# Optimization experiments

Hardware: AMD Instinct MI355X
Metric: run time of the kernel (lower is better)

## Reference

```python
import jax, jax.numpy as jnp
import numpy as np

# Dims (match init_kwargs / input_specs)
B, S, HID = 1, 2048, 2048
NH, NKV, HD = 16, 4, 128          # head_dim = HID // NH
REP = NH // NKV                    # num_key_value_groups
BLOCK_SIZE, LOCAL_BLOCKS, SINK_NUM = 8, 4, 4
SCALING = HD ** -0.5


def rotate_half(x):
    x1, x2 = jnp.split(x, 2, axis=-1)
    return jnp.concatenate([-x2, x1], axis=-1)


def setup_inputs() -> dict:
    key = jax.random.key(0)
    ks = jax.random.split(key, 7)
    return {
        "hidden_states": jax.random.normal(ks[0], (B, S, HID), jnp.float32),
        "cos": jax.random.uniform(ks[1], (B, S, HD), jnp.float32, minval=-1.0, maxval=1.0),
        "sin": jax.random.uniform(ks[2], (B, S, HD), jnp.float32, minval=-1.0, maxval=1.0),
        # Projection weights stored as [in, out] so x @ W matches nn.Linear (bias=False).
        "Wq": 0.02 * jax.random.normal(ks[3], (HID, NH * HD), jnp.float32),
        "Wk": 0.02 * jax.random.normal(ks[4], (HID, NKV * HD), jnp.float32),
        "Wv": 0.02 * jax.random.normal(ks[5], (HID, NKV * HD), jnp.float32),
        "Wo": 0.02 * jax.random.normal(ks[6], (NH * HD, HID), jnp.float32),
    }


def sink_local_mask(seq_len):
    # query i attends to: sink tokens j < min(SINK_NUM, i), and local window
    # max(0, i - LOCAL_BLOCKS*BLOCK_SIZE) <= j <= i (diagonal included so every
    # row has at least one valid key; see notes).
    i = jnp.arange(seq_len)[:, None]
    j = jnp.arange(seq_len)[None, :]
    sink = j < jnp.minimum(SINK_NUM, i)
    local = (j >= i - LOCAL_BLOCKS * BLOCK_SIZE) & (j <= i)
    return sink | local  # [S, S] bool, broadcast over (B, H)


def reference(hidden_states, cos, sin, Wq, Wk, Wv, Wo):
    # projections -> [B, H, S, D]
    q = (hidden_states @ Wq).reshape(B, S, NH, HD).transpose(0, 2, 1, 3)
    k = (hidden_states @ Wk).reshape(B, S, NKV, HD).transpose(0, 2, 1, 3)
    v = (hidden_states @ Wv).reshape(B, S, NKV, HD).transpose(0, 2, 1, 3)
    # rotary embedding, cos/sin broadcast over head dim (unsqueeze_dim=1)
    c = cos[:, None, :, :]
    s = sin[:, None, :, :]
    q = q * c + rotate_half(q) * s
    k = k * c + rotate_half(k) * s
    # repeat_kv (GQA) -> [B, NH, S, D]
    k = jnp.repeat(k, REP, axis=1)
    v = jnp.repeat(v, REP, axis=1)
    # sink + local sparse attention (dense compute + mask, as in source)
    scores = jnp.einsum('bhqd,bhkd->bhqk', q, k) * SCALING
    mask = sink_local_mask(S)
    scores = jnp.where(mask, scores, -jnp.inf)
    attn_weights = jax.nn.softmax(scores, axis=-1)
    attn_output = jnp.einsum('bhqk,bhkd->bhqd', attn_weights, v)
    # Faithful to source: view(B, S, -1) on the [B, H, S, D] layout WITHOUT a
    # transpose(1,2) first (the original code omits it).
    attn_output = attn_output.reshape(B, S, NH * HD)
    attn_output = attn_output @ Wo
    return attn_output, attn_weights
```

## Files before the change

kernel.cpp:

```cpp
#include <hip/hip_runtime.h>

typedef unsigned short ushort_t;
typedef __attribute__((ext_vector_type(8))) short short8;
typedef __attribute__((ext_vector_type(4))) float f32x4;
typedef __attribute__((ext_vector_type(8))) unsigned short us8;
typedef __attribute__((ext_vector_type(4))) unsigned short us4;

#define SEQ 2048
#define HIDD 2048
#define XLD 3072
#define SCALING 0.08838834764831843f

__device__ __forceinline__ float bf2f(ushort_t u) {
    unsigned int x = ((unsigned int)u) << 16;
    return __builtin_bit_cast(float, x);
}
__device__ __forceinline__ ushort_t f2bf(float f) {
    unsigned int u = __builtin_bit_cast(unsigned int, f);
    u += 0x7fffu + ((u >> 16) & 1u);
    return (ushort_t)(u >> 16);
}

__device__ __forceinline__ void transpose_tile(
    const float* __restrict__ W, ushort_t* __restrict__ Wt,
    int N, int n0, int k0, int dstRow0) {
    __shared__ ushort_t t[64 * 80];
    const int tid = threadIdx.x;
    {
        const int kl = tid >> 4;
        const int nc = (tid & 15) * 4;
        #pragma unroll
        for (int p = 0; p < 4; ++p) {
            int k = kl + p * 16;
            float4 v = *(const float4*)(W + (size_t)(k0 + k) * N + n0 + nc);
            t[(nc + 0) * 80 + k] = f2bf(v.x);
            t[(nc + 1) * 80 + k] = f2bf(v.y);
            t[(nc + 2) * 80 + k] = f2bf(v.z);
            t[(nc + 3) * 80 + k] = f2bf(v.w);
        }
    }
    __syncthreads();
    {
        const int nl = tid >> 3;
        const int kc = (tid & 7) * 8;
        #pragma unroll
        for (int p = 0; p < 2; ++p) {
            int n = nl + p * 32;
            *(us8*)(Wt + (size_t)(dstRow0 + n) * HIDD + k0 + kc) =
                *(const us8*)&t[n * 80 + kc];
        }
    }
}

__global__ __launch_bounds__(256) void transpose_all(
    const float* __restrict__ Wq, const float* __restrict__ Wk,
    const float* __restrict__ Wv, const float* __restrict__ Wo,
    const float* __restrict__ hid,
    ushort_t* __restrict__ Wqkvt, ushort_t* __restrict__ Wot,
    ushort_t* __restrict__ Hb) {
    int bx = blockIdx.x, k0 = blockIdx.y * 64;
    if (bx < 32)       transpose_tile(Wq, Wqkvt, 2048, bx * 64,        k0, bx * 64);
    else if (bx < 40)  transpose_tile(Wk, Wqkvt, 512,  (bx - 32) * 64, k0, 2048 + (bx - 32) * 64);
    else if (bx < 48)  transpose_tile(Wv, Wqkvt, 512,  (bx - 40) * 64, k0, 2560 + (bx - 40) * 64);
    else if (bx < 80)  transpose_tile(Wo, Wot,   2048, (bx - 48) * 64, k0, (bx - 48) * 64);
    else {
        int chunk = (bx - 80) * 32 + blockIdx.y;
        size_t base = (size_t)chunk * 4096 + threadIdx.x * 16;
        #pragma unroll
        for (int p = 0; p < 4; ++p) {
            float4 v = *(const float4*)(hid + base + p * 4);
            us4 o;
            o[0] = f2bf(v.x); o[1] = f2bf(v.y); o[2] = f2bf(v.z); o[3] = f2bf(v.w);
            *(us4*)(Hb + base + p * 4) = o;
        }
    }
}

__global__ __launch_bounds__(256) void gemm_splitk(
    const ushort_t* __restrict__ A, int lda,
    const ushort_t* __restrict__ Bt, int ldb,
    ushort_t* __restrict__ P, int ldc,
    const int4 kexts) {
    __shared__ ushort_t lA[2 * 128 * 32];
    __shared__ ushort_t lB[2 * 128 * 32];
    const int tid = threadIdx.x;
    const int wave = tid >> 6, lane = tid & 63;
    const int wm = wave >> 1, wn = wave & 1;
    const int quad = lane >> 4, l16 = lane & 15;
    const int m0 = blockIdx.y * 128, n0 = blockIdx.x * 128;
    const int z = blockIdx.z;

    const int ke[4] = {kexts.x, kexts.y, kexts.z, kexts.w};
    int koff = 0;
    for (int zz = 0; zz < 4; ++zz) if (zz < z) koff += ke[zz];
    const int kext = ke[z];

    A  += (size_t)koff;
    Bt += (size_t)koff;
    P  += (size_t)z * ((size_t)gridDim.y * 128) * ldc;

    const int srow = lane >> 2;
    const int scol = 8 * ((lane & 3) ^ (srow & 3));

    f32x4 acc[4][4] = {};

    const ushort_t* Ab = A  + (size_t)(m0 + wave * 16 + srow) * lda + scol;
    const ushort_t* Bb = Bt + (size_t)(n0 + wave * 16 + srow) * ldb + scol;
    ushort_t* lAw = lA + (wave * 16) * 32;
    ushort_t* lBw = lB + (wave * 16) * 32;

    const int rsw = (quad ^ (l16 & 3)) * 8;

    for (int kk = 0; kk < kext; kk += 64) {
        __syncthreads();
        #pragma unroll
        for (int kh = 0; kh < 2; ++kh) {
            #pragma unroll
            for (int c = 0; c < 2; ++c) {
                __builtin_amdgcn_global_load_lds(
                    (const __attribute__((address_space(1))) unsigned int*)(const void*)
                        (Ab + (size_t)(c * 64) * lda + kk + kh * 32),
                    (__attribute__((address_space(3))) unsigned int*)(void*)
                        (lAw + kh * 128 * 32 + c * 64 * 32), 16, 0, 0);
                __builtin_amdgcn_global_load_lds(
                    (const __attribute__((address_space(1))) unsigned int*)(const void*)
                        (Bb + (size_t)(c * 64) * ldb + kk + kh * 32),
                    (__attribute__((address_space(3))) unsigned int*)(void*)
                        (lBw + kh * 128 * 32 + c * 64 * 32), 16, 0, 0);
            }
        }
        __syncthreads();
        #pragma unroll
        for (int kh = 0; kh < 2; ++kh) {
            short8 af[4], bfr[4];
            #pragma unroll
            for (int mt = 0; mt < 4; ++mt)
                af[mt] = *(const short8*)&lA[kh * 128 * 32 + (wm * 64 + mt * 16 + l16) * 32 + rsw];
            #pragma unroll
            for (int nt = 0; nt < 4; ++nt)
                bfr[nt] = *(const short8*)&lB[kh * 128 * 32 + (wn * 64 + nt * 16 + l16) * 32 + rsw];
            #pragma unroll
            for (int mt = 0; mt < 4; ++mt) {
                #pragma unroll
                for (int nt = 0; nt < 4; ++nt)
                    acc[mt][nt] = __builtin_amdgcn_mfma_f32_16x16x32_bf16(
                        af[mt], bfr[nt], acc[mt][nt], 0, 0, 0);
            }
        }
    }

    #pragma unroll
    for (int mt = 0; mt < 4; ++mt) {
        #pragma unroll
        for (int nt = 0; nt < 4; ++nt) {
            int gm = m0 + wm * 64 + mt * 16 + quad * 4;
            int gn = n0 + wn * 64 + nt * 16 + l16;
            #pragma unroll
            for (int r = 0; r < 4; ++r)
                P[(size_t)(gm + r) * ldc + gn] = f2bf(acc[mt][nt][r]);
        }
    }
}

#define RWAVES (SEQ * 10)
#define VWAVES (SEQ * 2)
__global__ __launch_bounds__(256) void reduce_x(
    const ushort_t* __restrict__ P, ushort_t* __restrict__ X,
    const float* __restrict__ cosp, const float* __restrict__ sinp) {
    const size_t ZS = (size_t)SEQ * XLD;
    int wid = blockIdx.x * 4 + (threadIdx.x >> 6);
    int lane = threadIdx.x & 63;
    if (wid < RWAVES) {
        int s = wid / 10, seg = wid % 10;
        int c0 = seg * 256 + lane * 4;
        size_t base = (size_t)s * XLD + c0;
        us4 a = *(const us4*)(P + base);
        us4 b = *(const us4*)(P + ZS + base);
        float x[4];
        #pragma unroll
        for (int t = 0; t < 4; ++t) x[t] = bf2f(a[t]) + bf2f(b[t]);
        float p[4];
        #pragma unroll
        for (int t = 0; t < 4; ++t) p[t] = __shfl_xor(x[t], 16, 64);
        int d = (lane * 4) & 127;
        float4 cv = *(const float4*)(cosp + (size_t)s * 128 + d);
        float4 sv = *(const float4*)(sinp + (size_t)s * 128 + d);
        float sgn = (lane & 16) ? 1.f : -1.f;
        us4 o;
        o[0] = f2bf(x[0] * cv.x + sgn * p[0] * sv.x);
        o[1] = f2bf(x[1] * cv.y + sgn * p[1] * sv.y);
        o[2] = f2bf(x[2] * cv.z + sgn * p[2] * sv.z);
        o[3] = f2bf(x[3] * cv.w + sgn * p[3] * sv.w);
        *(us4*)(X + base) = o;
    } else {
        int w2 = wid - RWAVES;
        int s = w2 >> 1;
        int c0 = 2560 + (w2 & 1) * 256 + lane * 4;
        size_t base = (size_t)s * XLD + c0;
        us4 a = *(const us4*)(P + base);
        us4 b = *(const us4*)(P + ZS + base);
        us4 o;
        #pragma unroll
        for (int t = 0; t < 4; ++t) o[t] = f2bf(bf2f(a[t]) + bf2f(b[t]));
        *(us4*)(X + base) = o;
    }
}

__global__ __launch_bounds__(256) void reduce_out3(
    const ushort_t* __restrict__ P, float* __restrict__ out) {
    const size_t ZS = (size_t)SEQ * HIDD;
    size_t idx = ((size_t)blockIdx.x * 256 + threadIdx.x) * 4;
    us4 a = *(const us4*)(P + idx);
    us4 b = *(const us4*)(P + ZS + idx);
    us4 c = *(const us4*)(P + 2 * ZS + idx);
    float4 o;
    o.x = bf2f(a[0]) + bf2f(b[0]) + bf2f(c[0]);
    o.y = bf2f(a[1]) + bf2f(b[1]) + bf2f(c[1]);
    o.z = bf2f(a[2]) + bf2f(b[2]) + bf2f(c[2]);
    o.w = bf2f(a[3]) + bf2f(b[3]) + bf2f(c[3]);
    *(float4*)(out + idx) = o;
}

__device__ __forceinline__ float qk_round(
    const ushort_t* __restrict__ Kbase, const float* qf,
    int jg, int dg, int lo, int nsink, int r) {
    int jj = r * 16 + jg;
    int j = (jj < nsink) ? jj : (lo + jj - nsink);
    if (j > SEQ - 1) j = SEQ - 1;
    const uint4* kp = (const uint4*)(Kbase + (size_t)j * XLD + dg * 32);
    float p = 0.f;
    #pragma unroll
    for (int pq = 0; pq < 4; ++pq) {
        uint4 v = kp[pq];
        unsigned int uu[4] = {v.x, v.y, v.z, v.w};
        #pragma unroll
        for (int t = 0; t < 4; ++t) {
            p += qf[pq * 8 + t * 2]     * bf2f((ushort_t)(uu[t] & 0xffffu));
            p += qf[pq * 8 + t * 2 + 1] * bf2f((ushort_t)(uu[t] >> 16));
        }
    }
    p += __shfl_xor(p, 1, 64);
    p += __shfl_xor(p, 2, 64);
    return p * SCALING;
}

__global__ __launch_bounds__(256) void attn_kernel(
    const ushort_t* __restrict__ X, float* __restrict__ Wts,
    ushort_t* __restrict__ Aout) {
    int g = blockIdx.x * 4 + (threadIdx.x >> 6);
    int lane = threadIdx.x & 63;
    int i = g & (SEQ - 1);
    int h = g >> 11;

    const int dg = lane & 3;
    const int jg = lane >> 2;

    const ushort_t* Q = X + (size_t)i * XLD + h * 128;
    float qf[32];
    {
        const uint4* qp = (const uint4*)(Q + dg * 32);
        #pragma unroll
        for (int p = 0; p < 4; ++p) {
            uint4 v = qp[p];
            unsigned int uu[4] = {v.x, v.y, v.z, v.w};
            #pragma unroll
            for (int t = 0; t < 4; ++t) {
                qf[p * 8 + t * 2]     = bf2f((ushort_t)(uu[t] & 0xffffu));
                qf[p * 8 + t * 2 + 1] = bf2f((ushort_t)(uu[t] >> 16));
            }
        }
    }

    int lo = i - 32; if (lo < 0) lo = 0;
    int nsink = lo < 4 ? lo : 4;
    int NJ = nsink + (i - lo + 1);

    const ushort_t* Kbase = X + 2048 + (h >> 2) * 128;
    const ushort_t* Vbase = X + 2560 + (h >> 2) * 128;

    float s0 = qk_round(Kbase, qf, jg, dg, lo, nsink, 0);
    float s1 = qk_round(Kbase, qf, jg, dg, lo, nsink, 1);
    float s2 = qk_round(Kbase, qf, jg, dg, lo, nsink, 2);

    int src = (lane & 15) * 4;
    float m0 = __shfl(s0, src, 64);
    float m1 = __shfl(s1, src, 64);
    float m2 = __shfl(s2, src, 64);
    float mysc = (lane < 16) ? m0 : ((lane < 32) ? m1 : m2);
    if (lane >= NJ) mysc = -1e30f;

    float m = mysc;
    #pragma unroll
    for (int off = 32; off > 0; off >>= 1) m = fmaxf(m, __shfl_xor(m, off, 64));

    float e = (lane < NJ) ? expf(mysc - m) : 0.f;
    float l = e;
    #pragma unroll
    for (int off = 32; off > 0; off >>= 1) l += __shfl_xor(l, off, 64);
    float w = e / l;

    float* row = Wts + ((size_t)h * SEQ + i) * SEQ;
    #pragma unroll
    for (int s = 0; s < 8; ++s) {
        float4 o;
        #pragma unroll
        for (int t = 0; t < 4; ++t) {
            int c = s * 256 + lane * 4 + t;
            bool in = (c < nsink) || (c >= lo && c <= i);
            int jjc = in ? ((c < nsink) ? c : (nsink + c - lo)) : 0;
            float wv = __shfl(w, jjc, 64);
            o[t] = in ? wv : 0.f;
        }
        *(float4*)(row + s * 256 + lane * 4) = o;
    }

    float o0 = 0.f, o1 = 0.f;
    for (int jj = 0; jj < NJ; ++jj) {
        int j = (jj < nsink) ? jj : (lo + jj - nsink);
        float pb = __shfl(w, jj, 64);
        unsigned int vv = *(const unsigned int*)(Vbase + (size_t)j * XLD + 2 * lane);
        o0 += pb * bf2f((ushort_t)(vv & 0xffff));
        o1 += pb * bf2f((ushort_t)(vv >> 16));
    }
    int r = h * 128 + (i >> 4);
    int c = (i & 15) * 128 + 2 * lane;
    ushort_t* Ar = Aout + (size_t)r * HIDD + c;
    Ar[0] = f2bf(o0);
    Ar[1] = f2bf(o1);
}

extern "C" void kernel_launch(void* const* d_in, const int* in_sizes, int n_in,
                              void* d_out, int out_size, void* d_ws, size_t ws_size,
                              hipStream_t stream) {
    if (n_in < 7) return;
    const float* hid  = (const float*)d_in[0];
    const float* cosp = (const float*)d_in[1];
    const float* sinp = (const float*)d_in[2];
    const float* Wq   = (const float*)d_in[3];
    const float* Wk   = (const float*)d_in[4];
    const float* Wv   = (const float*)d_in[5];
    const float* Wo   = (const float*)d_in[6];

    float* out = (float*)d_out;
    float* wts = out + (size_t)SEQ * HIDD;

    ushort_t* Hb    = (ushort_t*)d_ws;
    ushort_t* Wqkvt = Hb    + (size_t)2048 * 2048;
    ushort_t* Wot   = Wqkvt + (size_t)3072 * 2048;
    ushort_t* X     = Wot   + (size_t)2048 * 2048;
    ushort_t* Am    = X     + (size_t)SEQ * XLD;
    ushort_t* Pqkv  = Am    + (size_t)SEQ * HIDD;
    ushort_t* Pout  = Pqkv  + 2 * (size_t)SEQ * XLD;
    size_t need = ((char*)(Pout + 3 * (size_t)SEQ * HIDD)) - (char*)d_ws;
    if (ws_size < need) return;

    dim3 blk(256);
    transpose_all<<<dim3(112, 32), blk, 0, stream>>>(
        Wq, Wk, Wv, Wo, hid, Wqkvt, Wot, Hb);

    gemm_splitk<<<dim3(24, 16, 2), blk, 0, stream>>>(
        Hb, HIDD, Wqkvt, 2048, Pqkv, XLD, make_int4(1024, 1024, 0, 0));
    reduce_x<<<(RWAVES + VWAVES) / 4, blk, 0, stream>>>(
        Pqkv, X, cosp, sinp);

    attn_kernel<<<(SEQ * 16) / 4, blk, 0, stream>>>(X, wts, Am);

    gemm_splitk<<<dim3(16, 16, 3), blk, 0, stream>>>(
        Am, HIDD, Wot, 2048, Pout, HIDD, make_int4(704, 704, 640, 0));
    reduce_out3<<<(SEQ * HIDD) / (256 * 4), blk, 0, stream>>>(Pout, out);
}
```

Baseline: 492.3 us.

## Stage shared K/V window in LDS for blocks of 16 queries

```diff
diff --git a/kernel.cpp b/kernel.cpp
--- a/kernel.cpp
+++ b/kernel.cpp
@@ -221,23 +221,25 @@
     *(float4*)(out + idx) = o;
 }
 
-__device__ __forceinline__ float qk_round(
-    const ushort_t* __restrict__ Kbase, const float* qf,
-    int jg, int dg, int lo, int nsink, int r) {
+#define SMLD 136
+__device__ __forceinline__ float qk_round_lds(
+    const ushort_t* __restrict__ sm, const float* qf,
+    int jg, int dg, int lo, int nsink, int w0, int r) {
     int jj = r * 16 + jg;
-    int j = (jj < nsink) ? jj : (lo + jj - nsink);
-    if (j > SEQ - 1) j = SEQ - 1;
-    const uint4* kp = (const uint4*)(Kbase + (size_t)j * XLD + dg * 32);
+    int row;
+    if (jj < nsink) row = 48 + jj;
+    else {
+        int widx = lo + jj - nsink - w0;
+        if (widx > 47) widx = 47;
+        row = widx;
+    }
+    const ushort_t* kp = sm + row * SMLD + dg * 32;
     float p = 0.f;
     #pragma unroll
     for (int pq = 0; pq < 4; ++pq) {
-        uint4 v = kp[pq];
-        unsigned int uu[4] = {v.x, v.y, v.z, v.w};
-        #pragma unroll
-        for (int t = 0; t < 4; ++t) {
-            p += qf[pq * 8 + t * 2]     * bf2f((ushort_t)(uu[t] & 0xffffu));
-            p += qf[pq * 8 + t * 2 + 1] * bf2f((ushort_t)(uu[t] >> 16));
-        }
+        us8 v = *(const us8*)(kp + pq * 8);
+        #pragma unroll
+        for (int t = 0; t < 8; ++t) p += qf[pq * 8 + t] * bf2f(v[t]);
     }
     p += __shfl_xor(p, 1, 64);
     p += __shfl_xor(p, 2, 64);
@@ -247,86 +249,106 @@
 __global__ __launch_bounds__(256) void attn_kernel(
     const ushort_t* __restrict__ X, float* __restrict__ Wts,
     ushort_t* __restrict__ Aout) {
-    int g = blockIdx.x * 4 + (threadIdx.x >> 6);
-    int lane = threadIdx.x & 63;
-    int i = g & (SEQ - 1);
-    int h = g >> 11;
+    __shared__ ushort_t sm[104 * SMLD];
+    const int tid = threadIdx.x;
+    const int lane = tid & 63;
+    const int wv = tid >> 6;
+    const int h = blockIdx.x >> 7;
+    const int i0 = (blockIdx.x & 127) << 4;
+    const int w0 = (i0 >= 32) ? (i0 - 32) : 0;
+    const int kvh = h >> 2;
+
+    const ushort_t* Kg = X + 2048 + kvh * 128;
+    const ushort_t* Vg = X + 2560 + kvh * 128;
+
+    #pragma unroll
+    for (int p = 0; p < 7; ++p) {
+        int tau = p * 16 + (tid >> 4);
+        if (tau < 104) {
+            int rr = (tau < 52) ? tau : (tau - 52);
+            int grow = (rr < 48) ? (w0 + rr) : (rr - 48);
+            const ushort_t* src = ((tau < 52) ? Kg : Vg) + (size_t)grow * XLD + (tid & 15) * 8;
+            *(us8*)&sm[tau * SMLD + (tid & 15) * 8] = *(const us8*)src;
+        }
+    }
+    __syncthreads();
 
     const int dg = lane & 3;
     const int jg = lane >> 2;
 
-    const ushort_t* Q = X + (size_t)i * XLD + h * 128;
-    float qf[32];
-    {
-        const uint4* qp = (const uint4*)(Q + dg * 32);
-        #pragma unroll
-        for (int p = 0; p < 4; ++p) {
-            uint4 v = qp[p];
-            unsigned int uu[4] = {v.x, v.y, v.z, v.w};
+    for (int ii = 0; ii < 4; ++ii) {
+        const int i = i0 + wv * 4 + ii;
+
+        float qf[32];
+        {
+            const ushort_t* Q = X + (size_t)i * XLD + h * 128 + dg * 32;
+            #pragma unroll
+            for (int pq = 0; pq < 4; ++pq) {
+                us8 v = *(const us8*)(Q + pq * 8);
+                #pragma unroll
+                for (int t = 0; t < 8; ++t) qf[pq * 8 + t] = bf2f(v[t]);
+            }
+        }
+
+        int lo = i - 32; if (lo < 0) lo = 0;
+        int nsink = lo < 4 ? lo : 4;
+        int NJ = nsink + (i - lo + 1);
+
+        float s0 = qk_round_lds(sm, qf, jg, dg, lo, nsink, w0, 0);
+        float s1 = qk_round_lds(sm, qf, jg, dg, lo, nsink, w0, 1);
+        float s2 = qk_round_lds(sm, qf, jg, dg, lo, nsink, w0, 2);
+
+        int src = (lane & 15) * 4;
+        float m0 = __shfl(s0, src, 64);
+        float m1 = __shfl(s1, src, 64);
+        float m2 = __shfl(s2, src, 64);
+        float mysc = (lane < 16) ? m0 : ((lane < 32) ? m1 : m2);
+        if (lane >= NJ) mysc = -1e30f;
+
+        float m = mysc;
+        #pragma unroll
+        for (int off = 32; off > 0; off >>= 1) m = fmaxf(m, __shfl_xor(m, off, 64));
+
+        float e = (lane < NJ) ? expf(mysc - m) : 0.f;
+        float l = e;
+        #pragma unroll
+        for (int off = 32; off > 0; off >>= 1) l += __shfl_xor(l, off, 64);
+        float w = e / l;
+
+        float* row = Wts + ((size_t)h * SEQ + i) * SEQ;
+        #pragma unroll
+        for (int s = 0; s < 8; ++s) {
+            float4 o;
             #pragma unroll
             for (int t = 0; t < 4; ++t) {
-                qf[p * 8 + t * 2]     = bf2f((ushort_t)(uu[t] & 0xffffu));
-                qf[p * 8 + t * 2 + 1] = bf2f((ushort_t)(uu[t] >> 16));
-            }
-        }
-    }
-
-    int lo = i - 32; if (lo < 0) lo = 0;
-    int nsink = lo < 4 ? lo : 4;
-    int NJ = nsink + (i - lo + 1);
-
-    const ushort_t* Kbase = X + 2048 + (h >> 2) * 128;
-    const ushort_t* Vbase = X + 2560 + (h >> 2) * 128;
-
-    float s0 = qk_round(Kbase, qf, jg, dg, lo, nsink, 0);
-    float s1 = qk_round(Kbase, qf, jg, dg, lo, nsink, 1);
-    float s2 = qk_round(Kbase, qf, jg, dg, lo, nsink, 2);
-
-    int src = (lane & 15) * 4;
-    float m0 = __shfl(s0, src, 64);
-    float m1 = __shfl(s1, src, 64);
-    float m2 = __shfl(s2, src, 64);
-    float mysc = (lane < 16) ? m0 : ((lane < 32) ? m1 : m2);
-    if (lane >= NJ) mysc = -1e30f;
-
-    float m = mysc;
-    #pragma unroll
-    for (int off = 32; off > 0; off >>= 1) m = fmaxf(m, __shfl_xor(m, off, 64));
-
-    float e = (lane < NJ) ? expf(mysc - m) : 0.f;
-    float l = e;
-    #pragma unroll
-    for (int off = 32; off > 0; off >>= 1) l += __shfl_xor(l, off, 64);
-    float w = e / l;
-
-    float* row = Wts + ((size_t)h * SEQ + i) * SEQ;
-    #pragma unroll
-    for (int s = 0; s < 8; ++s) {
-        float4 o;
-        #pragma unroll
-        for (int t = 0; t < 4; ++t) {
-            int c = s * 256 + lane * 4 + t;
-            bool in = (c < nsink) || (c >= lo && c <= i);
-            int jjc = in ? ((c < nsink) ? c : (nsink + c - lo)) : 0;
-            float wv = __shfl(w, jjc, 64);
-            o[t] = in ? wv : 0.f;
-        }
-        *(float4*)(row + s * 256 + lane * 4) = o;
-    }
-
-    float o0 = 0.f, o1 = 0.f;
-    for (int jj = 0; jj < NJ; ++jj) {
-        int j = (jj < nsink) ? jj : (lo + jj - nsink);
-        float pb = __shfl(w, jj, 64);
-        unsigned int vv = *(const unsigned int*)(Vbase + (size_t)j * XLD + 2 * lane);
-        o0 += pb * bf2f((ushort_t)(vv & 0xffff));
-        o1 += pb * bf2f((ushort_t)(vv >> 16));
-    }
-    int r = h * 128 + (i >> 4);
-    int c = (i & 15) * 128 + 2 * lane;
-    ushort_t* Ar = Aout + (size_t)r * HIDD + c;
-    Ar[0] = f2bf(o0);
-    Ar[1] = f2bf(o1);
+                int c = s * 256 + lane * 4 + t;
+                bool in = (c < nsink) || (c >= lo && c <= i);
+                int jjc = in ? ((c < nsink) ? c : (nsink + c - lo)) : 0;
+                float wv2 = __shfl(w, jjc, 64);
+                o[t] = in ? wv2 : 0.f;
+            }
+            *(float4*)(row + s * 256 + lane * 4) = o;
+        }
+
+        float o0 = 0.f, o1 = 0.f;
+        for (int jj = 0; jj < NJ; ++jj) {
+            int vrow;
+            if (jj < nsink) vrow = 100 + jj;
+            else {
+                int widx = lo + jj - nsink - w0;
+                vrow = 52 + widx;
+            }
+            float pb = __shfl(w, jj, 64);
+            unsigned int vv = *(const unsigned int*)&sm[vrow * SMLD + 2 * lane];
+            o0 += pb * bf2f((ushort_t)(vv & 0xffff));
+            o1 += pb * bf2f((ushort_t)(vv >> 16));
+        }
+        int r = h * 128 + (i >> 4);
+        int c = (i & 15) * 128 + 2 * lane;
+        ushort_t* Ar = Aout + (size_t)r * HIDD + c;
+        Ar[0] = f2bf(o0);
+        Ar[1] = f2bf(o1);
+    }
 }
 
 extern "C" void kernel_launch(void* const* d_in, const int* in_sizes, int n_in,
@@ -363,7 +385,7 @@
     reduce_x<<<(RWAVES + VWAVES) / 4, blk, 0, stream>>>(
         Pqkv, X, cosp, sinp);
 
-    attn_kernel<<<(SEQ * 16) / 4, blk, 0, stream>>>(X, wts, Am);
+    attn_kernel<<<SEQ * 16 / 16, blk, 0, stream>>>(X, wts, Am);
 
     gemm_splitk<<<dim3(16, 16, 3), blk, 0, stream>>>(
         Am, HIDD, Wot, 2048, Pout, HIDD, make_int4(704, 704, 640, 0));
```

Measured after the change: 448.9 us (median of 2 runs). -8.8%, faster.
